# Kernel optimization log

Hardware: AMD Instinct MI355X
Metric: run time of the kernel (lower is better)

## Reference

```python
import jax, jax.numpy as jnp
import numpy as np
from jax import lax

DIM = 512; NUM_HEADS = 8; WS = 2; POOL = 3
HEAD_DIM = DIM // NUM_HEADS
L_HEADS = int(NUM_HEADS * 0.5); L_DIM = L_HEADS * HEAD_DIM
H_HEADS = NUM_HEADS - L_HEADS; H_DIM = H_HEADS * HEAD_DIM
SCALE = HEAD_DIM ** (-0.5)


def setup_inputs():
    key = jax.random.key(0)
    ks = jax.random.split(key, 8)
    B, Hh, Ww = 8, 64, 64
    N = Hh * Ww
    s = lambda fan: 1.0 / np.sqrt(fan)
    return {
        'x': jax.random.normal(ks[0], (B, N, DIM), jnp.float32),
        'H': Hh,
        'l_q_w': jax.random.normal(ks[1], (DIM, L_DIM), jnp.float32) * s(DIM),
        'l_kv_w': jax.random.normal(ks[2], (DIM, 2 * L_DIM), jnp.float32) * s(DIM),
        'l_proj_w': jax.random.normal(ks[3], (L_DIM, L_DIM), jnp.float32) * s(L_DIM),
        'l_proj_b': jax.random.normal(ks[4], (L_DIM,), jnp.float32) * 0.01,
        'h_qkv_w': jax.random.normal(ks[5], (DIM, H_DIM), jnp.float32) * s(DIM),
        'h_proj_w': jax.random.normal(ks[6], (H_DIM, H_DIM), jnp.float32) * s(H_DIM),
        'h_proj_b': jax.random.normal(ks[7], (H_DIM,), jnp.float32) * 0.01,
    }


def _avgpool3_same(x):
    # x: [M, ws, ws, C]; 3x3 avg pool, stride 1, pad 1, count_include_pad=False
    ssum = lax.reduce_window(x, jnp.float32(0.0), lax.add,
                             (1, POOL, POOL, 1), (1, 1, 1, 1),
                             ((0, 0), (1, 1), (1, 1), (0, 0)))
    ones = jnp.ones(x.shape[1:3], x.dtype)
    cnt = lax.reduce_window(ones, jnp.float32(0.0), lax.add,
                            (POOL, POOL), (1, 1), ((1, 1), (1, 1)))
    return ssum / cnt[None, :, :, None]


def _hifi(x, h_qkv_w, h_proj_w, h_proj_b):
    B, H, W, C = x.shape
    hg, wg = H // WS, W // WS
    x = x @ h_qkv_w  # [B,H,W,H_DIM]
    # partition into ws x ws windows: [B*hg*wg, ws, ws, H_DIM]
    xw = x.reshape(B, hg, WS, wg, WS, H_DIM).transpose(0, 1, 3, 2, 4, 5)
    xw = xw.reshape(B * hg * wg, WS, WS, H_DIM)
    xw = _avgpool3_same(xw) - xw
    xw = xw.reshape(B, hg, wg, WS, WS, H_DIM).transpose(0, 1, 3, 2, 4, 5)
    xw = xw.reshape(B, H, W, H_DIM)
    return xw @ h_proj_w + h_proj_b


def _lofi(x, l_q_w, l_kv_w, l_proj_w, l_proj_b):
    B, H, W, C = x.shape
    q = (x @ l_q_w).reshape(B, H * W, L_HEADS, HEAD_DIM).transpose(0, 2, 1, 3)
    # spatial reduction: avg pool ws stride ws -> [B, H/ws * W/ws, C]
    xp = x.reshape(B, H // WS, WS, W // WS, WS, C).mean(axis=(2, 4))
    xp = xp.reshape(B, -1, C)
    kv = (xp @ l_kv_w).reshape(B, -1, 2, L_HEADS, HEAD_DIM)
    k = kv[:, :, 0].transpose(0, 2, 1, 3)  # [B,h,M,d]
    v = kv[:, :, 1].transpose(0, 2, 1, 3)
    attn = jax.nn.softmax(jnp.einsum('bhnd,bhmd->bhnm', q, k) * SCALE, axis=-1)
    out = jnp.einsum('bhnm,bhmd->bhnd', attn, v)
    out = out.transpose(0, 2, 1, 3).reshape(B, H, W, L_DIM)
    return out @ l_proj_w + l_proj_b


def reference(x, H, l_q_w, l_kv_w, l_proj_w, l_proj_b, h_qkv_w, h_proj_w, h_proj_b):
    B, N, C = x.shape
    W = N // H
    xg = x.reshape(B, H, W, C)
    hi = _hifi(xg, h_qkv_w, h_proj_w, h_proj_b)
    lo = _lofi(xg, l_q_w, l_kv_w, l_proj_w, l_proj_b)
    out = jnp.concatenate([hi, lo], axis=-1)  # [B,H,W,C]
    return out.reshape(B, N, C)
```

## Files before the change

### kernel.cpp

```cpp
#include <hip/hip_runtime.h>

typedef __bf16 bf16x8 __attribute__((ext_vector_type(8)));
typedef float  f32x4  __attribute__((ext_vector_type(4)));
typedef unsigned int u32x4 __attribute__((ext_vector_type(4)));
typedef unsigned short u16x8 __attribute__((ext_vector_type(8)));
typedef unsigned short u16x4 __attribute__((ext_vector_type(4)));

__device__ __forceinline__ unsigned short f2bf(float f) {
    return __builtin_bit_cast(unsigned short, (__bf16)f);
}
__device__ __forceinline__ float bf2f(unsigned short s) {
    return (float)__builtin_bit_cast(__bf16, s);
}
__device__ __forceinline__ bf16x8 as_bf16x8(u32x4 v) {
    return __builtin_bit_cast(bf16x8, v);
}

#define AS1 __attribute__((address_space(1)))
#define AS3 __attribute__((address_space(3)))
__device__ __forceinline__ void gload_lds16(const void* g, void* l) {
    __builtin_amdgcn_global_load_lds((const AS1 void*)g, (AS3 void*)l, 16, 0, 0);
}


__global__ __launch_bounds__(256) void k_cast_x(const float* __restrict__ x,
                                                unsigned short* __restrict__ xb) {
    int i = blockIdx.x * 256 + threadIdx.x;
    f32x4 v = ((const f32x4*)x)[i];
    u16x4 o = { f2bf(v[0]), f2bf(v[1]), f2bf(v[2]), f2bf(v[3]) };
    ((u16x4*)xb)[i] = o;
}

__global__ __launch_bounds__(256) void k_pool(const unsigned short* __restrict__ xb,
                                              unsigned short* __restrict__ xpb) {
    int t = blockIdx.x * 256 + threadIdx.x;
    int r = t >> 6, c8 = (t & 63) << 3;
    int b = r >> 10, hw = r & 1023;
    int h2 = hw >> 5, w2 = hw & 31;
    int n00 = (h2 << 7) + (w2 << 1);
    const unsigned short* base = xb + ((size_t)(b << 12) + n00) * 512 + c8;
    u16x8 v0 = *(const u16x8*)base;
    u16x8 v1 = *(const u16x8*)(base + 512);
    u16x8 v2 = *(const u16x8*)(base + 64 * 512);
    u16x8 v3 = *(const u16x8*)(base + 65 * 512);
    u16x8 o;
#pragma unroll
    for (int j = 0; j < 8; j++)
        o[j] = f2bf(0.25f * (bf2f(v0[j]) + bf2f(v1[j]) + bf2f(v2[j]) + bf2f(v3[j])));
    *(u16x8*)(xpb + (size_t)r * 512 + c8) = o;
}

__global__ __launch_bounds__(256) void k_weights(
        const float* __restrict__ h_qkv_w, const float* __restrict__ l_q_w,
        const float* __restrict__ l_kv_w, const float* __restrict__ h_proj_w,
        const float* __restrict__ l_proj_w,
        unsigned short* __restrict__ wcatT, unsigned short* __restrict__ lkvT,
        unsigned short* __restrict__ hprojT, unsigned short* __restrict__ lprojT) {
    int i = blockIdx.x * 256 + threadIdx.x;
    if (i < 262144) {
        int n = i >> 9, k = i & 511;
        float v = (n < 256) ? h_qkv_w[k * 256 + n] : l_q_w[k * 256 + (n - 256)];
        wcatT[i] = f2bf(v);
    } else if (i < 524288) {
        int j = i - 262144; int n = j >> 9, k = j & 511;
        lkvT[j] = f2bf(l_kv_w[k * 512 + n]);
    } else if (i < 589824) {
        int j = i - 524288; int n = j >> 8, k = j & 255;
        hprojT[j] = f2bf(h_proj_w[k * 256 + n]);
    } else {
        int j = i - 589824; int n = j >> 8, k = j & 255;
        lprojT[j] = f2bf(l_proj_w[k * 256 + n]);
    }
}

__global__ __launch_bounds__(256) void k_vt(const unsigned short* __restrict__ kvm,
                                            unsigned short* __restrict__ vT) {
    int t = blockIdx.x * 256 + threadIdx.x;
    int bh = t >> 13;
    int rem = t & 8191;
    int ck = rem >> 6;
    int d = rem & 63;
    int b = bh >> 2, h = bh & 3;
    const unsigned short* src = kvm + ((size_t)(b * 1024 + ck * 8)) * 512 + 256 + h * 64 + d;
    u16x8 v;
#pragma unroll
    for (int j = 0; j < 8; j++) v[j] = src[j * 512];
    *(u16x8*)(vT + ((size_t)(bh * 64 + d)) * 1024 + ck * 8) = v;
}

__global__ __launch_bounds__(256) void k_hifi(const unsigned short* __restrict__ hqq,
                                              unsigned short* __restrict__ dbuf) {
    int t = blockIdx.x * 256 + threadIdx.x;
    int win = t >> 5, c8 = (t & 31) << 3;
    int b = win >> 10, wi = win & 1023;
    int h2 = wi >> 5, w2 = wi & 31;
    int n00 = (b << 12) + (h2 << 7) + (w2 << 1);
    const unsigned short* p = hqq + (size_t)n00 * 512 + c8;
    u16x8 a0 = *(const u16x8*)p;
    u16x8 a1 = *(const u16x8*)(p + 512);
    u16x8 a2 = *(const u16x8*)(p + 64 * 512);
    u16x8 a3 = *(const u16x8*)(p + 65 * 512);
    u16x8 o0, o1, o2, o3;
#pragma unroll
    for (int j = 0; j < 8; j++) {
        float f0 = bf2f(a0[j]), f1 = bf2f(a1[j]), f2 = bf2f(a2[j]), f3 = bf2f(a3[j]);
        float m = 0.25f * (f0 + f1 + f2 + f3);
        o0[j] = f2bf(m - f0); o1[j] = f2bf(m - f1);
        o2[j] = f2bf(m - f2); o3[j] = f2bf(m - f3);
    }
    unsigned short* q = dbuf + (size_t)n00 * 256 + c8;
    *(u16x8*)q = o0;
    *(u16x8*)(q + 256) = o1;
    *(u16x8*)(q + 64 * 256) = o2;
    *(u16x8*)(q + 65 * 256) = o3;
}

__global__ __launch_bounds__(256, 2) void k_gemm(
        const unsigned short* __restrict__ A,
        const unsigned short* __restrict__ Bt,
        unsigned short* __restrict__ Cb,
        float* __restrict__ Cf,
        const float* __restrict__ bias,
        int K, int ldc, int coloff) {
    __shared__ __align__(16) unsigned short As[128 * 32];
    __shared__ __align__(16) unsigned short Bs[128 * 32];
    const int tid = threadIdx.x;
    const int wave = tid >> 6, lane = tid & 63;
    const int m16 = lane & 15, quad = lane >> 4;
    const int wr = wave >> 1, wc = wave & 1;
    const size_t row0 = (size_t)blockIdx.x * 128;
    const int col0 = blockIdx.y * 128;

    const int srow = lane >> 2;
    const int scol = (lane & 3) * 8;
    const unsigned short* Ap0 = A + (row0 + wave * 32 + srow) * (size_t)K + scol;
    const unsigned short* Ap1 = Ap0 + (size_t)16 * K;
    const unsigned short* Bp0 = Bt + (size_t)(col0 + wave * 32 + srow) * K + scol;
    const unsigned short* Bp1 = Bp0 + (size_t)16 * K;
    unsigned short* Al0 = As + wave * 1024;
    unsigned short* Al1 = As + wave * 1024 + 512;
    unsigned short* Bl0 = Bs + wave * 1024;
    unsigned short* Bl1 = Bs + wave * 1024 + 512;

    f32x4 acc[4][4] = {};

    for (int k0 = 0; k0 < K; k0 += 32) {
        __syncthreads();
        gload_lds16(Ap0 + k0, Al0);
        gload_lds16(Ap1 + k0, Al1);
        gload_lds16(Bp0 + k0, Bl0);
        gload_lds16(Bp1 + k0, Bl1);
        __syncthreads();
        bf16x8 af[4], bfr[4];
#pragma unroll
        for (int mi = 0; mi < 4; mi++)
            af[mi] = as_bf16x8(*(const u32x4*)(As + (wr * 64 + mi * 16 + m16) * 32 + quad * 8));
#pragma unroll
        for (int ni = 0; ni < 4; ni++)
            bfr[ni] = as_bf16x8(*(const u32x4*)(Bs + (wc * 64 + ni * 16 + m16) * 32 + quad * 8));
#pragma unroll
        for (int mi = 0; mi < 4; mi++)
#pragma unroll
            for (int ni = 0; ni < 4; ni++)
                acc[mi][ni] = __builtin_amdgcn_mfma_f32_16x16x32_bf16(af[mi], bfr[ni], acc[mi][ni], 0, 0, 0);
    }

#pragma unroll
    for (int mi = 0; mi < 4; mi++) {
#pragma unroll
        for (int ni = 0; ni < 4; ni++) {
            const int colL = col0 + wc * 64 + ni * 16 + m16;
            const float bv = bias ? bias[colL] : 0.0f;
#pragma unroll
            for (int r = 0; r < 4; r++) {
                const size_t row = row0 + wr * 64 + mi * 16 + quad * 4 + r;
                float v = acc[mi][ni][r] + bv;
                if (Cf) Cf[row * ldc + coloff + colL] = v;
                else    Cb[row * ldc + coloff + colL] = f2bf(v);
            }
        }
    }
}

__global__ __launch_bounds__(512, 4) void k_attn(
        const unsigned short* __restrict__ hqq,
        const unsigned short* __restrict__ kvm,
        const unsigned short* __restrict__ vT,
        unsigned short* __restrict__ aout) {
    __shared__ __align__(16) unsigned short Kb[2][64 * 72];
    __shared__ __align__(16) unsigned short Vb[2][64 * 72];
    __shared__ __align__(16) unsigned short Pl[8][32 * 72];
    const int tid = threadIdx.x;
    const int wave = tid >> 6, lane = tid & 63;
    const int m16 = lane & 15, quad = lane >> 4;
    const int qtile = blockIdx.x, bh = blockIdx.y;
    const int b = bh >> 2, h = bh & 3;

    bf16x8 qf[2][2];
    const size_t qrow0 = (size_t)b * 4096 + qtile * 256 + wave * 32;
#pragma unroll
    for (int qh = 0; qh < 2; qh++) {
        const unsigned short* qp = hqq + (qrow0 + qh * 16 + m16) * 512 + 256 + h * 64 + quad * 8;
        qf[qh][0] = as_bf16x8(*(const u32x4*)qp);
        qf[qh][1] = as_bf16x8(*(const u32x4*)(qp + 32));
    }

    f32x4 o[2][4] = {};
    float lp[2] = {0.f, 0.f};

    const int sr = tid >> 3;
    const int sc = tid & 7;
    const unsigned short* kg = kvm + ((size_t)b * 1024) * 512 + h * 64 + sc * 8;
    const unsigned short* vg = vT + ((size_t)bh * 64) * 1024 + sc * 8;

    u32x4 stg0 = *(const u32x4*)(kg + (size_t)sr * 512);
    u32x4 stg1 = *(const u32x4*)(vg + (size_t)sr * 1024);
    *(u32x4*)&Kb[0][sr * 72 + sc * 8] = stg0;
    *(u32x4*)&Vb[0][sr * 72 + sc * 8] = stg1;

    for (int it = 0; it < 16; ++it) {
        const int cur = it & 1, nxt = cur ^ 1;
        __syncthreads();
        if (it + 1 < 16) {
            const size_t kvb = (size_t)(it + 1) * 64;
            stg0 = *(const u32x4*)(kg + (kvb + sr) * 512);
            stg1 = *(const u32x4*)(vg + kvb + (size_t)sr * 1024);
        }

#pragma unroll
        for (int mt = 0; mt < 4; mt++) {
            const unsigned short* kp = &Kb[cur][(mt * 16 + m16) * 72 + quad * 8];
            const bf16x8 kf0 = as_bf16x8(*(const u32x4*)kp);
            const bf16x8 kf1 = as_bf16x8(*(const u32x4*)(kp + 32));
            f32x4 st[2] = {};
#pragma unroll
            for (int qh = 0; qh < 2; qh++) {
                st[qh] = __builtin_amdgcn_mfma_f32_16x16x32_bf16(kf0, qf[qh][0], st[qh], 0, 0, 0);
                st[qh] = __builtin_amdgcn_mfma_f32_16x16x32_bf16(kf1, qf[qh][1], st[qh], 0, 0, 0);
            }
#pragma unroll
            for (int qh = 0; qh < 2; qh++) {
                float p0 = __expf(st[qh][0] * 0.125f);
                float p1 = __expf(st[qh][1] * 0.125f);
                float p2 = __expf(st[qh][2] * 0.125f);
                float p3 = __expf(st[qh][3] * 0.125f);
                lp[qh] += (p0 + p1) + (p2 + p3);
                u16x4 pk = { f2bf(p0), f2bf(p1), f2bf(p2), f2bf(p3) };
                *(u16x4*)&Pl[wave][(qh * 16 + m16) * 72 + mt * 16 + quad * 4] = pk;
            }
        }
        asm volatile("s_waitcnt lgkmcnt(0)" ::: "memory");

        bf16x8 pf[2][2];
#pragma unroll
        for (int qh = 0; qh < 2; qh++) {
            const unsigned short* pp = &Pl[wave][(qh * 16 + m16) * 72 + quad * 8];
            pf[qh][0] = as_bf16x8(*(const u32x4*)pp);
            pf[qh][1] = as_bf16x8(*(const u32x4*)(pp + 32));
        }
#pragma unroll
        for (int nt = 0; nt < 4; nt++) {
            const unsigned short* vp = &Vb[cur][(nt * 16 + m16) * 72 + quad * 8];
            const bf16x8 vf0 = as_bf16x8(*(const u32x4*)vp);
            const bf16x8 vf1 = as_bf16x8(*(const u32x4*)(vp + 32));
#pragma unroll
            for (int qh = 0; qh < 2; qh++) {
                o[qh][nt] = __builtin_amdgcn_mfma_f32_16x16x32_bf16(pf[qh][0], vf0, o[qh][nt], 0, 0, 0);
                o[qh][nt] = __builtin_amdgcn_mfma_f32_16x16x32_bf16(pf[qh][1], vf1, o[qh][nt], 0, 0, 0);
            }
        }

        if (it + 1 < 16) {
            *(u32x4*)&Kb[nxt][sr * 72 + sc * 8] = stg0;
            *(u32x4*)&Vb[nxt][sr * 72 + sc * 8] = stg1;
        }
    }

#pragma unroll
    for (int qh = 0; qh < 2; qh++) {
        float l = lp[qh];
        l += __shfl_xor(l, 16);
        l += __shfl_xor(l, 32);
        f32x4 linv;
#pragma unroll
        for (int r = 0; r < 4; r++)
            linv[r] = __builtin_amdgcn_rcpf(__shfl(l, quad * 4 + r));
#pragma unroll
        for (int nt = 0; nt < 4; nt++)
#pragma unroll
            for (int r = 0; r < 4; r++)
                aout[(qrow0 + qh * 16 + quad * 4 + r) * 256 + h * 64 + nt * 16 + m16] =
                    f2bf(o[qh][nt][r] * linv[r]);
    }
}


extern "C" void kernel_launch(void* const* d_in, const int* in_sizes, int n_in,
                              void* d_out, int out_size, void* d_ws, size_t ws_size,
                              hipStream_t stream) {
    (void)in_sizes; (void)n_in; (void)out_size; (void)ws_size;
    const float* x        = (const float*)d_in[0];
    const float* l_q_w    = (const float*)d_in[2];
    const float* l_kv_w   = (const float*)d_in[3];
    const float* l_proj_w = (const float*)d_in[4];
    const float* l_proj_b = (const float*)d_in[5];
    const float* h_qkv_w  = (const float*)d_in[6];
    const float* h_proj_w = (const float*)d_in[7];
    const float* h_proj_b = (const float*)d_in[8];
    float* out = (float*)d_out;

    char* ws = (char*)d_ws;
    unsigned short* xb     = (unsigned short*)(ws);
    unsigned short* dbuf   = (unsigned short*)(ws);
    unsigned short* aout   = (unsigned short*)(ws + 16777216);
    unsigned short* xpb    = (unsigned short*)(ws + 33554432);
    unsigned short* vTbuf  = (unsigned short*)(ws + 33554432);
    unsigned short* wcatT  = (unsigned short*)(ws + 41943040);
    unsigned short* lkvT   = (unsigned short*)(ws + 42467328);
    unsigned short* hprojT = (unsigned short*)(ws + 42991616);
    unsigned short* lprojT = (unsigned short*)(ws + 43122688);
    unsigned short* hqq    = (unsigned short*)(ws + 43253760);
    unsigned short* kvm    = (unsigned short*)(ws + 76808192);

    k_cast_x <<<16384, 256, 0, stream>>>(x, xb);
    k_pool   <<<2048,  256, 0, stream>>>(xb, xpb);
    k_weights<<<2560,  256, 0, stream>>>(h_qkv_w, l_q_w, l_kv_w, h_proj_w, l_proj_w,
                                         wcatT, lkvT, hprojT, lprojT);
    k_gemm<<<dim3(256, 4), 256, 0, stream>>>(xb, wcatT, hqq, nullptr, nullptr, 512, 512, 0);
    k_gemm<<<dim3(64, 4), 256, 0, stream>>>(xpb, lkvT, kvm, nullptr, nullptr, 512, 512, 0);
    k_vt<<<1024, 256, 0, stream>>>(kvm, vTbuf);
    k_hifi<<<1024, 256, 0, stream>>>(hqq, dbuf);
    k_gemm<<<dim3(256, 2), 256, 0, stream>>>(dbuf, hprojT, nullptr, out, h_proj_b, 256, 512, 0);
    k_attn<<<dim3(16, 32), 512, 0, stream>>>(hqq, kvm, vTbuf, aout);
    k_gemm<<<dim3(256, 2), 256, 0, stream>>>(aout, lprojT, nullptr, out, l_proj_b, 256, 512, 256);
}
```

Baseline: 265.4 us.

## Reorder tokens window-major and fuse prep, hifi, V-transpose and projections into four kernels

The bf16 cast of x now writes rows in 2x2-window-major order and is merged with pooling and weight transposition into a single prep kernel. With that ordering, the hifi window mean-minus-self runs in the first GEMM's epilogue, and the V transpose moves into the KV GEMM epilogue. The two input GEMMs share one launch, and so do the two output projections; the projection epilogue scatters rows back to spatial order. Attention now runs 4 waves of 64 query rows over separate q/k buffers. The aim is to cut launches and remove the intermediate round trips through hqq/kvm, at the cost of scattered epilogue stores and higher register pressure in attention.

Result: faster. 256.0 us (-3.6%).

```diff
diff --git a/kernel.cpp b/kernel.cpp
--- a/kernel.cpp
+++ b/kernel.cpp
@@ -23,114 +23,72 @@
 }
 
 
-__global__ __launch_bounds__(256) void k_cast_x(const float* __restrict__ x,
-                                                unsigned short* __restrict__ xb) {
-    int i = blockIdx.x * 256 + threadIdx.x;
-    f32x4 v = ((const f32x4*)x)[i];
-    u16x4 o = { f2bf(v[0]), f2bf(v[1]), f2bf(v[2]), f2bf(v[3]) };
-    ((u16x4*)xb)[i] = o;
-}
-
-__global__ __launch_bounds__(256) void k_pool(const unsigned short* __restrict__ xb,
-                                              unsigned short* __restrict__ xpb) {
-    int t = blockIdx.x * 256 + threadIdx.x;
-    int r = t >> 6, c8 = (t & 63) << 3;
-    int b = r >> 10, hw = r & 1023;
-    int h2 = hw >> 5, w2 = hw & 31;
-    int n00 = (h2 << 7) + (w2 << 1);
-    const unsigned short* base = xb + ((size_t)(b << 12) + n00) * 512 + c8;
-    u16x8 v0 = *(const u16x8*)base;
-    u16x8 v1 = *(const u16x8*)(base + 512);
-    u16x8 v2 = *(const u16x8*)(base + 64 * 512);
-    u16x8 v3 = *(const u16x8*)(base + 65 * 512);
-    u16x8 o;
-#pragma unroll
-    for (int j = 0; j < 8; j++)
-        o[j] = f2bf(0.25f * (bf2f(v0[j]) + bf2f(v1[j]) + bf2f(v2[j]) + bf2f(v3[j])));
-    *(u16x8*)(xpb + (size_t)r * 512 + c8) = o;
-}
-
-__global__ __launch_bounds__(256) void k_weights(
+__global__ __launch_bounds__(256) void k_prep(
+        const float* __restrict__ x,
         const float* __restrict__ h_qkv_w, const float* __restrict__ l_q_w,
         const float* __restrict__ l_kv_w, const float* __restrict__ h_proj_w,
         const float* __restrict__ l_proj_w,
+        unsigned short* __restrict__ xb, unsigned short* __restrict__ xpb,
         unsigned short* __restrict__ wcatT, unsigned short* __restrict__ lkvT,
         unsigned short* __restrict__ hprojT, unsigned short* __restrict__ lprojT) {
-    int i = blockIdx.x * 256 + threadIdx.x;
-    if (i < 262144) {
-        int n = i >> 9, k = i & 511;
-        float v = (n < 256) ? h_qkv_w[k * 256 + n] : l_q_w[k * 256 + (n - 256)];
-        wcatT[i] = f2bf(v);
-    } else if (i < 524288) {
-        int j = i - 262144; int n = j >> 9, k = j & 511;
-        lkvT[j] = f2bf(l_kv_w[k * 512 + n]);
-    } else if (i < 589824) {
-        int j = i - 524288; int n = j >> 8, k = j & 255;
-        hprojT[j] = f2bf(h_proj_w[k * 256 + n]);
+    int blk = blockIdx.x;
+    if (blk < 8192) {
+        int t = blk * 256 + threadIdx.x;
+        int row = t >> 6, c8 = (t & 63) << 3;
+        int b = row >> 12, nn = row & 4095;
+        int hh = nn >> 6, ww = nn & 63;
+        int mp = (((b << 10) + ((hh >> 1) << 5) + (ww >> 1)) << 2) + ((hh & 1) << 1) + (ww & 1);
+        const float* src = x + (size_t)row * 512 + c8;
+        f32x4 v0 = *(const f32x4*)src;
+        f32x4 v1 = *(const f32x4*)(src + 4);
+        u16x8 o = { f2bf(v0[0]), f2bf(v0[1]), f2bf(v0[2]), f2bf(v0[3]),
+                    f2bf(v1[0]), f2bf(v1[1]), f2bf(v1[2]), f2bf(v1[3]) };
+        *(u16x8*)(xb + (size_t)mp * 512 + c8) = o;
+    } else if (blk < 10240) {
+        int t = (blk - 8192) * 256 + threadIdx.x;
+        int r = t >> 6, c8 = (t & 63) << 3;
+        int b = r >> 10, hw = r & 1023;
+        int h2 = hw >> 5, w2 = hw & 31;
+        const float* base = x + ((size_t)(b << 12) + (h2 << 7) + (w2 << 1)) * 512 + c8;
+        u16x8 o;
+#pragma unroll
+        for (int half = 0; half < 2; half++) {
+            f32x4 a0 = *(const f32x4*)(base + half * 4);
+            f32x4 a1 = *(const f32x4*)(base + 512 + half * 4);
+            f32x4 a2 = *(const f32x4*)(base + 64 * 512 + half * 4);
+            f32x4 a3 = *(const f32x4*)(base + 65 * 512 + half * 4);
+            f32x4 m = (a0 + a1 + a2 + a3) * 0.25f;
+#pragma unroll
+            for (int j = 0; j < 4; j++) o[half * 4 + j] = f2bf(m[j]);
+        }
+        *(u16x8*)(xpb + (size_t)r * 512 + c8) = o;
     } else {
-        int j = i - 589824; int n = j >> 8, k = j & 255;
-        lprojT[j] = f2bf(l_proj_w[k * 256 + n]);
-    }
-}
-
-__global__ __launch_bounds__(256) void k_vt(const unsigned short* __restrict__ kvm,
-                                            unsigned short* __restrict__ vT) {
-    int t = blockIdx.x * 256 + threadIdx.x;
-    int bh = t >> 13;
-    int rem = t & 8191;
-    int ck = rem >> 6;
-    int d = rem & 63;
-    int b = bh >> 2, h = bh & 3;
-    const unsigned short* src = kvm + ((size_t)(b * 1024 + ck * 8)) * 512 + 256 + h * 64 + d;
-    u16x8 v;
-#pragma unroll
-    for (int j = 0; j < 8; j++) v[j] = src[j * 512];
-    *(u16x8*)(vT + ((size_t)(bh * 64 + d)) * 1024 + ck * 8) = v;
-}
-
-__global__ __launch_bounds__(256) void k_hifi(const unsigned short* __restrict__ hqq,
-                                              unsigned short* __restrict__ dbuf) {
-    int t = blockIdx.x * 256 + threadIdx.x;
-    int win = t >> 5, c8 = (t & 31) << 3;
-    int b = win >> 10, wi = win & 1023;
-    int h2 = wi >> 5, w2 = wi & 31;
-    int n00 = (b << 12) + (h2 << 7) + (w2 << 1);
-    const unsigned short* p = hqq + (size_t)n00 * 512 + c8;
-    u16x8 a0 = *(const u16x8*)p;
-    u16x8 a1 = *(const u16x8*)(p + 512);
-    u16x8 a2 = *(const u16x8*)(p + 64 * 512);
-    u16x8 a3 = *(const u16x8*)(p + 65 * 512);
-    u16x8 o0, o1, o2, o3;
-#pragma unroll
-    for (int j = 0; j < 8; j++) {
-        float f0 = bf2f(a0[j]), f1 = bf2f(a1[j]), f2 = bf2f(a2[j]), f3 = bf2f(a3[j]);
-        float m = 0.25f * (f0 + f1 + f2 + f3);
-        o0[j] = f2bf(m - f0); o1[j] = f2bf(m - f1);
-        o2[j] = f2bf(m - f2); o3[j] = f2bf(m - f3);
-    }
-    unsigned short* q = dbuf + (size_t)n00 * 256 + c8;
-    *(u16x8*)q = o0;
-    *(u16x8*)(q + 256) = o1;
-    *(u16x8*)(q + 64 * 256) = o2;
-    *(u16x8*)(q + 65 * 256) = o3;
-}
-
-__global__ __launch_bounds__(256, 2) void k_gemm(
-        const unsigned short* __restrict__ A,
-        const unsigned short* __restrict__ Bt,
-        unsigned short* __restrict__ Cb,
-        float* __restrict__ Cf,
-        const float* __restrict__ bias,
-        int K, int ldc, int coloff) {
-    __shared__ __align__(16) unsigned short As[128 * 32];
-    __shared__ __align__(16) unsigned short Bs[128 * 32];
+        int i = (blk - 10240) * 256 + threadIdx.x;
+        if (i < 262144) {
+            int n = i >> 9, k = i & 511;
+            float v = (n < 256) ? h_qkv_w[k * 256 + n] : l_q_w[k * 256 + (n - 256)];
+            wcatT[i] = f2bf(v);
+        } else if (i < 524288) {
+            int j = i - 262144; int n = j >> 9, k = j & 511;
+            lkvT[j] = f2bf(l_kv_w[k * 512 + n]);
+        } else if (i < 589824) {
+            int j = i - 524288; int n = j >> 8, k = j & 255;
+            hprojT[j] = f2bf(h_proj_w[k * 256 + n]);
+        } else {
+            int j = i - 589824; int n = j >> 8, k = j & 255;
+            lprojT[j] = f2bf(l_proj_w[k * 256 + n]);
+        }
+    }
+}
+
+__device__ __forceinline__ void mm_core(
+        const unsigned short* __restrict__ A, const unsigned short* __restrict__ Bt,
+        size_t row0, int col0, int K,
+        unsigned short* As, unsigned short* Bs, f32x4 (&acc)[4][4]) {
     const int tid = threadIdx.x;
     const int wave = tid >> 6, lane = tid & 63;
     const int m16 = lane & 15, quad = lane >> 4;
     const int wr = wave >> 1, wc = wave & 1;
-    const size_t row0 = (size_t)blockIdx.x * 128;
-    const int col0 = blockIdx.y * 128;
-
     const int srow = lane >> 2;
     const int scol = (lane & 3) * 8;
     const unsigned short* Ap0 = A + (row0 + wave * 32 + srow) * (size_t)K + scol;
@@ -142,8 +100,6 @@
     unsigned short* Bl0 = Bs + wave * 1024;
     unsigned short* Bl1 = Bs + wave * 1024 + 512;
 
-    f32x4 acc[4][4] = {};
-
     for (int k0 = 0; k0 < K; k0 += 32) {
         __syncthreads();
         gload_lds16(Ap0 + k0, Al0);
@@ -164,67 +120,181 @@
             for (int ni = 0; ni < 4; ni++)
                 acc[mi][ni] = __builtin_amdgcn_mfma_f32_16x16x32_bf16(af[mi], bfr[ni], acc[mi][ni], 0, 0, 0);
     }
-
-#pragma unroll
-    for (int mi = 0; mi < 4; mi++) {
+}
+
+__global__ __launch_bounds__(256, 2) void k_mm512(
+        const unsigned short* __restrict__ xb, const unsigned short* __restrict__ xpb,
+        const unsigned short* __restrict__ wcatT, const unsigned short* __restrict__ lkvT,
+        unsigned short* __restrict__ dbuf, unsigned short* __restrict__ qbuf,
+        unsigned short* __restrict__ kbuf, unsigned short* __restrict__ vT) {
+    __shared__ __align__(16) unsigned short As[128 * 32];
+    __shared__ __align__(16) unsigned short Bs[128 * 32];
+    const int flat = blockIdx.x;
+    const bool isg1 = flat < 1024;
+    const unsigned short* A;
+    const unsigned short* Bt;
+    size_t row0; int col0;
+    if (isg1) { A = xb;  Bt = wcatT; row0 = (size_t)(flat >> 2) * 128; col0 = (flat & 3) * 128; }
+    else { int f = flat - 1024; A = xpb; Bt = lkvT; row0 = (size_t)(f >> 2) * 128; col0 = (f & 3) * 128; }
+
+    f32x4 acc[4][4] = {};
+    mm_core(A, Bt, row0, col0, 512, As, Bs, acc);
+
+    const int tid = threadIdx.x;
+    const int wave = tid >> 6, lane = tid & 63;
+    const int m16 = lane & 15, quad = lane >> 4;
+    const int wr = wave >> 1, wc = wave & 1;
+
+    if (isg1) {
+        if (col0 < 256) {
+#pragma unroll
+            for (int mi = 0; mi < 4; mi++)
+#pragma unroll
+                for (int ni = 0; ni < 4; ni++) {
+                    const int col = col0 + wc * 64 + ni * 16 + m16;
+                    const size_t mb = row0 + wr * 64 + mi * 16 + quad * 4;
+                    float v0 = acc[mi][ni][0], v1 = acc[mi][ni][1];
+                    float v2 = acc[mi][ni][2], v3 = acc[mi][ni][3];
+                    float m = 0.25f * ((v0 + v1) + (v2 + v3));
+                    dbuf[(mb + 0) * 256 + col] = f2bf(m - v0);
+                    dbuf[(mb + 1) * 256 + col] = f2bf(m - v1);
+                    dbuf[(mb + 2) * 256 + col] = f2bf(m - v2);
+                    dbuf[(mb + 3) * 256 + col] = f2bf(m - v3);
+                }
+        } else {
+#pragma unroll
+            for (int mi = 0; mi < 4; mi++)
+#pragma unroll
+                for (int ni = 0; ni < 4; ni++) {
+                    const int col = col0 - 256 + wc * 64 + ni * 16 + m16;
+                    const size_t mb = row0 + wr * 64 + mi * 16 + quad * 4;
+#pragma unroll
+                    for (int r = 0; r < 4; r++)
+                        qbuf[(mb + r) * 256 + col] = f2bf(acc[mi][ni][r]);
+                }
+        }
+    } else {
+        if (col0 < 256) {
+#pragma unroll
+            for (int mi = 0; mi < 4; mi++)
+#pragma unroll
+                for (int ni = 0; ni < 4; ni++) {
+                    const int col = col0 + wc * 64 + ni * 16 + m16;
+                    const size_t row = row0 + wr * 64 + mi * 16 + quad * 4;
+#pragma unroll
+                    for (int r = 0; r < 4; r++)
+                        kbuf[(row + r) * 256 + col] = f2bf(acc[mi][ni][r]);
+                }
+        } else {
+#pragma unroll
+            for (int mi = 0; mi < 4; mi++)
+#pragma unroll
+                for (int ni = 0; ni < 4; ni++) {
+                    const int d = col0 - 256 + wc * 64 + ni * 16 + m16;
+                    const int hh = d >> 6, dd = d & 63;
+                    const size_t kvg = row0 + wr * 64 + mi * 16 + quad * 4;
+                    const int b = (int)(kvg >> 10), kv = (int)(kvg & 1023);
+                    u16x4 pk = { f2bf(acc[mi][ni][0]), f2bf(acc[mi][ni][1]),
+                                 f2bf(acc[mi][ni][2]), f2bf(acc[mi][ni][3]) };
+                    *(u16x4*)(vT + (((size_t)(b * 4 + hh) * 64 + dd) << 10) + kv) = pk;
+                }
+        }
+    }
+}
+
+__global__ __launch_bounds__(256, 2) void k_mmproj(
+        const unsigned short* __restrict__ dbuf, const unsigned short* __restrict__ aout,
+        const unsigned short* __restrict__ hprojT, const unsigned short* __restrict__ lprojT,
+        const float* __restrict__ h_proj_b, const float* __restrict__ l_proj_b,
+        float* __restrict__ out) {
+    __shared__ __align__(16) unsigned short As[128 * 32];
+    __shared__ __align__(16) unsigned short Bs[128 * 32];
+    const int flat = blockIdx.x;
+    const bool hi = flat < 512;
+    const int f = flat & 511;
+    const unsigned short* A  = hi ? dbuf : aout;
+    const unsigned short* Bt = hi ? hprojT : lprojT;
+    const float* bias = hi ? h_proj_b : l_proj_b;
+    const int coloff = hi ? 0 : 256;
+    const size_t row0 = (size_t)(f >> 1) * 128;
+    const int col0 = (f & 1) * 128;
+
+    f32x4 acc[4][4] = {};
+    mm_core(A, Bt, row0, col0, 256, As, Bs, acc);
+
+    const int tid = threadIdx.x;
+    const int wave = tid >> 6, lane = tid & 63;
+    const int m16 = lane & 15, quad = lane >> 4;
+    const int wr = wave >> 1, wc = wave & 1;
+
+#pragma unroll
+    for (int mi = 0; mi < 4; mi++)
 #pragma unroll
         for (int ni = 0; ni < 4; ni++) {
-            const int colL = col0 + wc * 64 + ni * 16 + m16;
-            const float bv = bias ? bias[colL] : 0.0f;
-#pragma unroll
-            for (int r = 0; r < 4; r++) {
-                const size_t row = row0 + wr * 64 + mi * 16 + quad * 4 + r;
-                float v = acc[mi][ni][r] + bv;
-                if (Cf) Cf[row * ldc + coloff + colL] = v;
-                else    Cb[row * ldc + coloff + colL] = f2bf(v);
-            }
-        }
-    }
-}
-
-__global__ __launch_bounds__(512, 4) void k_attn(
-        const unsigned short* __restrict__ hqq,
-        const unsigned short* __restrict__ kvm,
+            const int col = col0 + wc * 64 + ni * 16 + m16;
+            const float bv = bias[col];
+            const size_t mb = row0 + wr * 64 + mi * 16 + quad * 4;
+            const int widx = (int)(mb >> 2);
+            const int b = widx >> 10, rem = widx & 1023;
+            const int h2 = rem >> 5, w2 = rem & 31;
+            const size_t nb = ((size_t)b << 12) + (h2 << 7) + (w2 << 1);
+            float* op = out + nb * 512 + coloff + col;
+            op[0]            = acc[mi][ni][0] + bv;
+            op[512]          = acc[mi][ni][1] + bv;
+            op[64 * 512]     = acc[mi][ni][2] + bv;
+            op[65 * 512]     = acc[mi][ni][3] + bv;
+        }
+}
+
+__global__ __launch_bounds__(256, 2) void k_attn(
+        const unsigned short* __restrict__ qbuf,
+        const unsigned short* __restrict__ kbuf,
         const unsigned short* __restrict__ vT,
         unsigned short* __restrict__ aout) {
     __shared__ __align__(16) unsigned short Kb[2][64 * 72];
     __shared__ __align__(16) unsigned short Vb[2][64 * 72];
-    __shared__ __align__(16) unsigned short Pl[8][32 * 72];
+    __shared__ __align__(16) unsigned short Pl[4][64 * 72];
     const int tid = threadIdx.x;
     const int wave = tid >> 6, lane = tid & 63;
     const int m16 = lane & 15, quad = lane >> 4;
     const int qtile = blockIdx.x, bh = blockIdx.y;
     const int b = bh >> 2, h = bh & 3;
 
-    bf16x8 qf[2][2];
-    const size_t qrow0 = (size_t)b * 4096 + qtile * 256 + wave * 32;
-#pragma unroll
-    for (int qh = 0; qh < 2; qh++) {
-        const unsigned short* qp = hqq + (qrow0 + qh * 16 + m16) * 512 + 256 + h * 64 + quad * 8;
+    bf16x8 qf[4][2];
+    const size_t qrow0 = (size_t)b * 4096 + qtile * 256 + wave * 64;
+#pragma unroll
+    for (int qh = 0; qh < 4; qh++) {
+        const unsigned short* qp = qbuf + (qrow0 + qh * 16 + m16) * 256 + h * 64 + quad * 8;
         qf[qh][0] = as_bf16x8(*(const u32x4*)qp);
         qf[qh][1] = as_bf16x8(*(const u32x4*)(qp + 32));
     }
 
-    f32x4 o[2][4] = {};
-    float lp[2] = {0.f, 0.f};
+    f32x4 o[4][4] = {};
+    float lp[4] = {0.f, 0.f, 0.f, 0.f};
 
     const int sr = tid >> 3;
     const int sc = tid & 7;
-    const unsigned short* kg = kvm + ((size_t)b * 1024) * 512 + h * 64 + sc * 8;
+    const unsigned short* kg = kbuf + ((size_t)b * 1024) * 256 + h * 64 + sc * 8;
     const unsigned short* vg = vT + ((size_t)bh * 64) * 1024 + sc * 8;
 
-    u32x4 stg0 = *(const u32x4*)(kg + (size_t)sr * 512);
-    u32x4 stg1 = *(const u32x4*)(vg + (size_t)sr * 1024);
-    *(u32x4*)&Kb[0][sr * 72 + sc * 8] = stg0;
-    *(u32x4*)&Vb[0][sr * 72 + sc * 8] = stg1;
+    u32x4 s0 = *(const u32x4*)(kg + (size_t)sr * 256);
+    u32x4 s1 = *(const u32x4*)(kg + (size_t)(sr + 32) * 256);
+    u32x4 s2 = *(const u32x4*)(vg + (size_t)sr * 1024);
+    u32x4 s3 = *(const u32x4*)(vg + (size_t)(sr + 32) * 1024);
+    *(u32x4*)&Kb[0][sr * 72 + sc * 8] = s0;
+    *(u32x4*)&Kb[0][(sr + 32) * 72 + sc * 8] = s1;
+    *(u32x4*)&Vb[0][sr * 72 + sc * 8] = s2;
+    *(u32x4*)&Vb[0][(sr + 32) * 72 + sc * 8] = s3;
 
     for (int it = 0; it < 16; ++it) {
         const int cur = it & 1, nxt = cur ^ 1;
         __syncthreads();
         if (it + 1 < 16) {
             const size_t kvb = (size_t)(it + 1) * 64;
-            stg0 = *(const u32x4*)(kg + (kvb + sr) * 512);
-            stg1 = *(const u32x4*)(vg + kvb + (size_t)sr * 1024);
+            s0 = *(const u32x4*)(kg + (kvb + sr) * 256);
+            s1 = *(const u32x4*)(kg + (kvb + sr + 32) * 256);
+            s2 = *(const u32x4*)(vg + kvb + (size_t)sr * 1024);
+            s3 = *(const u32x4*)(vg + kvb + (size_t)(sr + 32) * 1024);
         }
 
 #pragma unroll
@@ -232,14 +302,14 @@
             const unsigned short* kp = &Kb[cur][(mt * 16 + m16) * 72 + quad * 8];
             const bf16x8 kf0 = as_bf16x8(*(const u32x4*)kp);
             const bf16x8 kf1 = as_bf16x8(*(const u32x4*)(kp + 32));
-            f32x4 st[2] = {};
-#pragma unroll
-            for (int qh = 0; qh < 2; qh++) {
+            f32x4 st[4] = {};
+#pragma unroll
+            for (int qh = 0; qh < 4; qh++) {
                 st[qh] = __builtin_amdgcn_mfma_f32_16x16x32_bf16(kf0, qf[qh][0], st[qh], 0, 0, 0);
                 st[qh] = __builtin_amdgcn_mfma_f32_16x16x32_bf16(kf1, qf[qh][1], st[qh], 0, 0, 0);
             }
 #pragma unroll
-            for (int qh = 0; qh < 2; qh++) {
+            for (int qh = 0; qh < 4; qh++) {
                 float p0 = __expf(st[qh][0] * 0.125f);
                 float p1 = __expf(st[qh][1] * 0.125f);
                 float p2 = __expf(st[qh][2] * 0.125f);
@@ -251,9 +321,9 @@
         }
         asm volatile("s_waitcnt lgkmcnt(0)" ::: "memory");
 
-        bf16x8 pf[2][2];
-#pragma unroll
-        for (int qh = 0; qh < 2; qh++) {
+        bf16x8 pf[4][2];
+#pragma unroll
+        for (int qh = 0; qh < 4; qh++) {
             const unsigned short* pp = &Pl[wave][(qh * 16 + m16) * 72 + quad * 8];
             pf[qh][0] = as_bf16x8(*(const u32x4*)pp);
             pf[qh][1] = as_bf16x8(*(const u32x4*)(pp + 32));
@@ -264,20 +334,22 @@
             const bf16x8 vf0 = as_bf16x8(*(const u32x4*)vp);
             const bf16x8 vf1 = as_bf16x8(*(const u32x4*)(vp + 32));
 #pragma unroll
-            for (int qh = 0; qh < 2; qh++) {
+            for (int qh = 0; qh < 4; qh++) {
                 o[qh][nt] = __builtin_amdgcn_mfma_f32_16x16x32_bf16(pf[qh][0], vf0, o[qh][nt], 0, 0, 0);
                 o[qh][nt] = __builtin_amdgcn_mfma_f32_16x16x32_bf16(pf[qh][1], vf1, o[qh][nt], 0, 0, 0);
             }
         }
 
         if (it + 1 < 16) {
-            *(u32x4*)&Kb[nxt][sr * 72 + sc * 8] = stg0;
-            *(u32x4*)&Vb[nxt][sr * 72 + sc * 8] = stg1;
-        }
-    }
-
-#pragma unroll
-    for (int qh = 0; qh < 2; qh++) {
+            *(u32x4*)&Kb[nxt][sr * 72 + sc * 8] = s0;
+            *(u32x4*)&Kb[nxt][(sr + 32) * 72 + sc * 8] = s1;
+            *(u32x4*)&Vb[nxt][sr * 72 + sc * 8] = s2;
+            *(u32x4*)&Vb[nxt][(sr + 32) * 72 + sc * 8] = s3;
+        }
+    }
+
+#pragma unroll
+    for (int qh = 0; qh < 4; qh++) {
         float l = lp[qh];
         l += __shfl_xor(l, 16);
         l += __shfl_xor(l, 32);
@@ -311,26 +383,20 @@
 
     char* ws = (char*)d_ws;
     unsigned short* xb     = (unsigned short*)(ws);
-    unsigned short* dbuf   = (unsigned short*)(ws);
-    unsigned short* aout   = (unsigned short*)(ws + 16777216);
-    unsigned short* xpb    = (unsigned short*)(ws + 33554432);
-    unsigned short* vTbuf  = (unsigned short*)(ws + 33554432);
-    unsigned short* wcatT  = (unsigned short*)(ws + 41943040);
-    unsigned short* lkvT   = (unsigned short*)(ws + 42467328);
-    unsigned short* hprojT = (unsigned short*)(ws + 42991616);
-    unsigned short* lprojT = (unsigned short*)(ws + 43122688);
-    unsigned short* hqq    = (unsigned short*)(ws + 43253760);
-    unsigned short* kvm    = (unsigned short*)(ws + 76808192);
-
-    k_cast_x <<<16384, 256, 0, stream>>>(x, xb);
-    k_pool   <<<2048,  256, 0, stream>>>(xb, xpb);
-    k_weights<<<2560,  256, 0, stream>>>(h_qkv_w, l_q_w, l_kv_w, h_proj_w, l_proj_w,
-                                         wcatT, lkvT, hprojT, lprojT);
-    k_gemm<<<dim3(256, 4), 256, 0, stream>>>(xb, wcatT, hqq, nullptr, nullptr, 512, 512, 0);
-    k_gemm<<<dim3(64, 4), 256, 0, stream>>>(xpb, lkvT, kvm, nullptr, nullptr, 512, 512, 0);
-    k_vt<<<1024, 256, 0, stream>>>(kvm, vTbuf);
-    k_hifi<<<1024, 256, 0, stream>>>(hqq, dbuf);
-    k_gemm<<<dim3(256, 2), 256, 0, stream>>>(dbuf, hprojT, nullptr, out, h_proj_b, 256, 512, 0);
-    k_attn<<<dim3(16, 32), 512, 0, stream>>>(hqq, kvm, vTbuf, aout);
-    k_gemm<<<dim3(256, 2), 256, 0, stream>>>(aout, lprojT, nullptr, out, l_proj_b, 256, 512, 256);
-}
+    unsigned short* aout   = (unsigned short*)(ws);
+    unsigned short* dbuf   = (unsigned short*)(ws + 33554432);
+    unsigned short* qbuf   = (unsigned short*)(ws + 50331648);
+    unsigned short* kbuf   = (unsigned short*)(ws + 67108864);
+    unsigned short* vT     = (unsigned short*)(ws + 71303168);
+    unsigned short* xpb    = (unsigned short*)(ws + 75497472);
+    unsigned short* wcatT  = (unsigned short*)(ws + 83886080);
+    unsigned short* lkvT   = (unsigned short*)(ws + 84410368);
+    unsigned short* hprojT = (unsigned short*)(ws + 84934656);
+    unsigned short* lprojT = (unsigned short*)(ws + 85065728);
+
+    k_prep<<<12800, 256, 0, stream>>>(x, h_qkv_w, l_q_w, l_kv_w, h_proj_w, l_proj_w,
+                                      xb, xpb, wcatT, lkvT, hprojT, lprojT);
+    k_mm512<<<1280, 256, 0, stream>>>(xb, xpb, wcatT, lkvT, dbuf, qbuf, kbuf, vT);
+    k_attn<<<dim3(16, 32), 256, 0, stream>>>(qbuf, kbuf, vT, aout);
+    k_mmproj<<<1024, 256, 0, stream>>>(dbuf, aout, hprojT, lprojT, h_proj_b, l_proj_b, out);
+}
```
